# Kernel optimization log

Measured on AMD Instinct MI355X. Metric: run time of the kernel, lower is better.

Reference implementation:

```python
import jax, jax.numpy as jnp
import numpy as np

DIM = 256
NHEADS = 4
HID = 512
B, H, W = 8, 48, 48
EPS = 1e-5


def _ln(x, g, b):
    mu = x.mean(-1, keepdims=True)
    var = ((x - mu) ** 2).mean(-1, keepdims=True)
    return (x - mu) * jax.lax.rsqrt(var + EPS) * g + b


def _mha(x, key_mask, wi, bi, wo, bo):
    # torch nn.MultiheadAttention (batch_first) with key padding restricted to active tokens
    Bn, N, C = x.shape
    hd = C // NHEADS
    qkv = x @ wi.T + bi  # [B,N,3C]
    q, k, v = jnp.split(qkv, 3, axis=-1)
    sh = lambda t: t.reshape(Bn, N, NHEADS, hd).transpose(0, 2, 1, 3)  # [B,h,N,hd]
    q, k, v = sh(q), sh(k), sh(v)
    scores = jnp.einsum('bhqd,bhkd->bhqk', q, k) / np.float32(np.sqrt(hd))
    scores = jnp.where(key_mask[:, None, None, :], scores, jnp.float32(-1e9))
    attn = jax.nn.softmax(scores, axis=-1)
    out = jnp.einsum('bhqk,bhkd->bhqd', attn, v)
    out = out.transpose(0, 2, 1, 3).reshape(Bn, N, C)
    return out @ wo.T + bo


def _mixer(x, key_mask, ln_g, ln_b, in_w, in_b, out_w, out_b, f1_w, f1_b, f2_w, f2_b):
    # MixerBlock: shared LayerNorm used before attn and before FFN
    xn = _ln(x, ln_g, ln_b)
    x = x + _mha(xn, key_mask, in_w, in_b, out_w, out_b)
    h = _ln(x, ln_g, ln_b)
    h = jax.nn.gelu(h @ f1_w.T + f1_b, approximate=False) @ f2_w.T + f2_b
    return x + h


def _forward(f_ir, f_vis, agent_w1, agent_b1, bn_gamma, bn_beta, bn_mean, bn_var,
             agent_w2, agent_b2, hyp_w1, hyp_b1, hyp_w2, hyp_b2,
             mir_ln_g, mir_ln_b, mir_in_w, mir_in_b, mir_out_w, mir_out_b,
             mir_f1_w, mir_f1_b, mir_f2_w, mir_f2_b,
             mvis_ln_g, mvis_ln_b, mvis_in_w, mvis_in_b, mvis_out_w, mvis_out_b,
             mvis_f1_w, mvis_f1_b, mvis_f2_w, mvis_f2_b, highlight_scale):
    Bn, C, Hh, Ww = f_ir.shape
    N = Hh * Ww
    base = f_ir + f_vis

    # SamplingAgent (1x1 convs as einsum, BatchNorm in eval mode)
    x = jnp.concatenate([f_ir, f_vis], axis=1)  # [B,2C,H,W]
    h = jnp.einsum('oc,bchw->bohw', agent_w1, x) + agent_b1[None, :, None, None]
    h = (h - bn_mean[None, :, None, None]) * jax.lax.rsqrt(bn_var[None, :, None, None] + EPS)
    h = h * bn_gamma[None, :, None, None] + bn_beta[None, :, None, None]
    h = jax.nn.relu(h)
    logits = jnp.einsum('oc,bchw->bohw', agent_w2, h) + agent_b2[None, :, None, None]
    w_driver = jax.nn.sigmoid(logits)  # [B,1,H,W]; eval path: driver = student

    # HyperNetwork threshold
    g = w_driver.mean(axis=(2, 3))  # [B,1]
    t = jax.nn.sigmoid(jax.nn.relu(g @ hyp_w1.T + hyp_b1) @ hyp_w2.T + hyp_b2)  # [B,1]

    wflat = w_driver.reshape(Bn, N)
    soft = jax.nn.sigmoid((wflat - t) * 50.0)  # [B,N]

    # active set: soft_mask > 0.5, fallback to top-64 of weights when too few
    active = soft > 0.5
    count = active.sum(axis=1)
    _, idx64 = jax.lax.top_k(wflat, 64)
    m64 = jnp.zeros((Bn, N), dtype=bool).at[jnp.arange(Bn)[:, None], idx64].set(True)
    active = jnp.where((count >= 64)[:, None], active, m64)

    tok_ir = f_ir.reshape(Bn, C, N).transpose(0, 2, 1)   # [B,N,C]
    tok_vis = f_vis.reshape(Bn, C, N).transpose(0, 2, 1)
    tok_base = base.reshape(Bn, C, N).transpose(0, 2, 1)

    refined_ir = _mixer(tok_ir, active, mir_ln_g, mir_ln_b, mir_in_w, mir_in_b,
                        mir_out_w, mir_out_b, mir_f1_w, mir_f1_b, mir_f2_w, mir_f2_b)
    refined_vis = _mixer(tok_vis, active, mvis_ln_g, mvis_ln_b, mvis_in_w, mvis_in_b,
                         mvis_out_w, mvis_out_b, mvis_f1_w, mvis_f1_b, mvis_f2_w, mvis_f2_b)

    wsel = wflat[..., None]
    fusion = refined_ir * wsel + refined_vis * (1.0 - wsel)
    delta = fusion * soft[..., None]
    mod = 1.0 + soft[..., None] * highlight_scale
    final = jnp.where(active[..., None], (tok_base + delta) * mod, tok_base)  # scatter-back
    f_final = final.transpose(0, 2, 1).reshape(Bn, C, Hh, Ww)
    aux_loss = jnp.float32(0.0)
    return f_final, aux_loss


def setup_inputs() -> dict:
    key = jax.random.key(0)
    ks = jax.random.split(key, 32)
    C = DIM
    S = 0.02
    r = lambda i, shape, s=S: jax.random.normal(ks[i], shape, dtype=jnp.float32) * s

    def mixer_params(prefix, k0):
        return {
            prefix + '_ln_g': jnp.ones((C,), jnp.float32),
            prefix + '_ln_b': jnp.zeros((C,), jnp.float32),
            prefix + '_in_w': r(k0, (3 * C, C)),
            prefix + '_in_b': jnp.zeros((3 * C,), jnp.float32),
            prefix + '_out_w': r(k0 + 1, (C, C)),
            prefix + '_out_b': jnp.zeros((C,), jnp.float32),
            prefix + '_f1_w': r(k0 + 2, (4 * C, C)),
            prefix + '_f1_b': jnp.zeros((4 * C,), jnp.float32),
            prefix + '_f2_w': r(k0 + 3, (C, 4 * C)),
            prefix + '_f2_b': jnp.zeros((C,), jnp.float32),
        }

    inp = {
        'f_ir': jax.random.normal(ks[0], (B, C, H, W), dtype=jnp.float32),
        'f_vis': jax.random.normal(ks[1], (B, C, H, W), dtype=jnp.float32),
        'agent_w1': r(2, (HID, 2 * C)),
        'agent_b1': jnp.zeros((HID,), jnp.float32),
        'bn_gamma': jnp.ones((HID,), jnp.float32),
        'bn_beta': jnp.zeros((HID,), jnp.float32),
        'bn_mean': jnp.zeros((HID,), jnp.float32),
        'bn_var': jnp.ones((HID,), jnp.float32),
        'agent_w2': r(3, (1, HID)),
        'agent_b2': jnp.zeros((1,), jnp.float32),
        'hyp_w1': r(4, (16, 1), 0.5),
        'hyp_b1': jnp.zeros((16,), jnp.float32),
        'hyp_w2': r(5, (1, 16), 0.5),
        'hyp_b2': jnp.zeros((1,), jnp.float32),
        'highlight_scale': jnp.float32(1.0),
    }
    inp.update(mixer_params('mir', 6))
    inp.update(mixer_params('mvis', 10))
    return inp


def reference(f_ir, f_vis, agent_w1, agent_b1, bn_gamma, bn_beta, bn_mean, bn_var,
              agent_w2, agent_b2, hyp_w1, hyp_b1, hyp_w2, hyp_b2,
              mir_ln_g, mir_ln_b, mir_in_w, mir_in_b, mir_out_w, mir_out_b,
              mir_f1_w, mir_f1_b, mir_f2_w, mir_f2_b,
              mvis_ln_g, mvis_ln_b, mvis_in_w, mvis_in_b, mvis_out_w, mvis_out_b,
              mvis_f1_w, mvis_f1_b, mvis_f2_w, mvis_f2_b, highlight_scale):
    return _forward(f_ir, f_vis, agent_w1, agent_b1, bn_gamma, bn_beta, bn_mean, bn_var,
                    agent_w2, agent_b2, hyp_w1, hyp_b1, hyp_w2, hyp_b2,
                    mir_ln_g, mir_ln_b, mir_in_w, mir_in_b, mir_out_w, mir_out_b,
                    mir_f1_w, mir_f1_b, mir_f2_w, mir_f2_b,
                    mvis_ln_g, mvis_ln_b, mvis_in_w, mvis_in_b, mvis_out_w, mvis_out_b,
                    mvis_f1_w, mvis_f1_b, mvis_f2_w, mvis_f2_b, highlight_scale)
```

## Files before the change

### kernel.cpp

```cpp
#include <hip/hip_runtime.h>
#include <hip/hip_bf16.h>
#include <cstdint>
#include <cstddef>

typedef __attribute__((ext_vector_type(8))) short short8;
typedef __attribute__((ext_vector_type(4))) short s16x4;
typedef __attribute__((ext_vector_type(4))) float f32x4;

#define DEVI static __device__ __forceinline__

constexpr int NB   = 8;
constexpr int CDIM = 256;
constexpr int NTOK = 2304;
constexpr int BNT  = NB * NTOK;
constexpr int HIDN = 512;
constexpr int RCAP = 2048;
constexpr size_t BNTC = (size_t)BNT * CDIM;
constexpr size_t KVSTR = (size_t)32 * NTOK * 64;
constexpr size_t HSTR  = (size_t)BNT * 1024;

DEVI unsigned short f2bf(float f) {
  unsigned u = __builtin_bit_cast(unsigned, f);
  unsigned r = 0x7FFFu + ((u >> 16) & 1u);
  return (unsigned short)((u + r) >> 16);
}
DEVI float bf2f(unsigned short h) {
  unsigned u = ((unsigned)h) << 16;
  return __builtin_bit_cast(float, u);
}

__global__ __launch_bounds__(256) void convert_weights(
    const float* __restrict__ miw, const float* __restrict__ mow,
    const float* __restrict__ mf1, const float* __restrict__ mf2,
    const float* __restrict__ viw, const float* __restrict__ vow,
    const float* __restrict__ vf1, const float* __restrict__ vf2,
    unsigned short* __restrict__ dst)
{
  int i = blockIdx.x * 256 + threadIdx.x;
  int m = i / 786432;
  int r = i % 786432;
  const float* src; int off;
  if      (r < 196608) { src = m ? viw : miw; off = r; }
  else if (r < 262144) { src = m ? vow : mow; off = r - 196608; }
  else if (r < 524288) { src = m ? vf1 : mf1; off = r - 262144; }
  else                 { src = m ? vf2 : mf2; off = r - 524288; }
  dst[i] = f2bf(src[off]);
}

__global__ __launch_bounds__(256) void split_w_kernel(
    const float* __restrict__ w1, unsigned short* __restrict__ W2)
{
  int i = blockIdx.x * 256 + threadIdx.x;
  int n = i >> 9, k = i & 511;
  float v = w1[i];
  unsigned short hi = f2bf(v);
  float r1 = v - bf2f(hi);
  unsigned short mid = f2bf(r1);
  size_t base = (size_t)n * 1024 + k;
  W2[base] = hi; W2[base + 512] = mid;
}

__global__ __launch_bounds__(256) void split_x_kernel(
    const float* __restrict__ f_ir, const float* __restrict__ f_vis,
    unsigned short* __restrict__ A2)
{
  __shared__ float tile[64][65];
  int n0 = blockIdx.x * 64, c0 = blockIdx.y * 64, b = blockIdx.z;
  int tid = threadIdx.x;
  const float* src = (c0 < 256) ? f_ir : f_vis;
  int cc0 = c0 & 255;
#pragma unroll
  for (int i = 0; i < 16; ++i) {
    int l = tid + i * 256;
    int r = l >> 6, col = l & 63;
    tile[r][col] = src[((size_t)b * 256 + cc0 + r) * NTOK + n0 + col];
  }
  __syncthreads();
#pragma unroll
  for (int i = 0; i < 16; ++i) {
    int l = tid + i * 256;
    int r = l >> 6, col = l & 63;
    float v = tile[col][r];
    unsigned short hi = f2bf(v);
    float r1 = v - bf2f(hi);
    unsigned short mid = f2bf(r1);
    size_t base = ((size_t)b * NTOK + n0 + r) * 1024 + c0 + col;
    A2[base] = hi; A2[base + 512] = mid;
  }
}

__global__ __launch_bounds__(256) void agent_gemm(
    const unsigned short* __restrict__ A2, const unsigned short* __restrict__ W2,
    const float* __restrict__ b1,
    const float* __restrict__ bng, const float* __restrict__ bnb,
    const float* __restrict__ bnm, const float* __restrict__ bnv,
    const float* __restrict__ w2, float* __restrict__ hpart)
{
  __shared__ unsigned short As[128][72];
  __shared__ unsigned short Ws[128][72];
  __shared__ float scl[64], shl[64], w2l[64];
  int tid = threadIdx.x;
  int lane = tid & 63, wid = tid >> 6;
  int wm = (wid >> 1) * 64, wn = (wid & 1) * 32;
  int m0 = blockIdx.x * 128, n0 = blockIdx.y * 64;
  if (tid < 64) {
    int n = n0 + tid;
    double inv = 1.0 / sqrt((double)bnv[n] + 1e-5);
    double sc = (double)bng[n] * inv;
    scl[tid] = (float)sc;
    shl[tid] = (float)(((double)b1[n] - (double)bnm[n]) * sc + (double)bnb[n]);
    w2l[tid] = w2[n];
  }
  f32x4 zero = {0.f, 0.f, 0.f, 0.f};
  f32x4 acc[4][2];
#pragma unroll
  for (int i = 0; i < 4; ++i)
#pragma unroll
    for (int j = 0; j < 2; ++j) acc[i][j] = zero;

  for (int kin = 0; kin < 512; kin += 64) {
    __syncthreads();
#pragma unroll
    for (int i = 0; i < 4; ++i) {
      int l = tid + i * 256;
      int r = l >> 3, ch = (l & 7) * 8;
      *(short8*)&As[r][ch] = *(const short8*)&A2[(size_t)(m0 + r) * 1024 + kin + ch];
    }
#pragma unroll
    for (int i = 0; i < 4; ++i) {
      int l = tid + i * 256;
      int r = l >> 3, ch = (l & 7) * 8;
      int wr = (r < 64) ? r : (r - 64);
      int wo = (r < 64) ? 0 : 512;
      *(short8*)&Ws[r][ch] = *(const short8*)&W2[(size_t)(n0 + wr) * 1024 + wo + kin + ch];
    }
    __syncthreads();
#pragma unroll
    for (int ks = 0; ks < 2; ++ks) {
      short8 a[4], bh[2], bm[2];
#pragma unroll
      for (int i = 0; i < 4; ++i)
        a[i] = *(const short8*)&As[wm + i * 16 + (lane & 15)][ks * 32 + (lane >> 4) * 8];
#pragma unroll
      for (int j = 0; j < 2; ++j) {
        bh[j] = *(const short8*)&Ws[wn + j * 16 + (lane & 15)][ks * 32 + (lane >> 4) * 8];
        bm[j] = *(const short8*)&Ws[64 + wn + j * 16 + (lane & 15)][ks * 32 + (lane >> 4) * 8];
      }
#pragma unroll
      for (int i = 0; i < 4; ++i)
#pragma unroll
        for (int j = 0; j < 2; ++j) {
          acc[i][j] = __builtin_amdgcn_mfma_f32_16x16x32_bf16(a[i], bh[j], acc[i][j], 0, 0, 0);
          acc[i][j] = __builtin_amdgcn_mfma_f32_16x16x32_bf16(a[i], bm[j], acc[i][j], 0, 0, 0);
        }
    }
  }
  for (int kin = 0; kin < 512; kin += 64) {
    __syncthreads();
#pragma unroll
    for (int i = 0; i < 4; ++i) {
      int l = tid + i * 256;
      int r = l >> 3, ch = (l & 7) * 8;
      *(short8*)&As[r][ch] = *(const short8*)&A2[(size_t)(m0 + r) * 1024 + 512 + kin + ch];
    }
#pragma unroll
    for (int i = 0; i < 2; ++i) {
      int l = tid + i * 256;
      int r = l >> 3, ch = (l & 7) * 8;
      *(short8*)&Ws[r][ch] = *(const short8*)&W2[(size_t)(n0 + r) * 1024 + kin + ch];
    }
    __syncthreads();
#pragma unroll
    for (int ks = 0; ks < 2; ++ks) {
      short8 a[4], bh[2];
#pragma unroll
      for (int i = 0; i < 4; ++i)
        a[i] = *(const short8*)&As[wm + i * 16 + (lane & 15)][ks * 32 + (lane >> 4) * 8];
#pragma unroll
      for (int j = 0; j < 2; ++j)
        bh[j] = *(const short8*)&Ws[wn + j * 16 + (lane & 15)][ks * 32 + (lane >> 4) * 8];
#pragma unroll
      for (int i = 0; i < 4; ++i)
#pragma unroll
        for (int j = 0; j < 2; ++j)
          acc[i][j] = __builtin_amdgcn_mfma_f32_16x16x32_bf16(a[i], bh[j], acc[i][j], 0, 0, 0);
    }
  }

  int rbase = (lane >> 4) * 4;
  int cbase = lane & 15;
  float part[4][4];
#pragma unroll
  for (int i = 0; i < 4; ++i) {
#pragma unroll
    for (int r = 0; r < 4; ++r) {
      float p = 0.f;
#pragma unroll
      for (int j = 0; j < 2; ++j) {
        int nl = wn + j * 16 + cbase;
        float val = acc[i][j][r] * scl[nl] + shl[nl];
        if (val > 0.f) p += val * w2l[nl];
      }
      part[i][r] = p;
    }
  }
#pragma unroll
  for (int msk = 1; msk < 16; msk <<= 1) {
#pragma unroll
    for (int i = 0; i < 4; ++i)
#pragma unroll
      for (int r = 0; r < 4; ++r)
        part[i][r] += __shfl_xor(part[i][r], msk);
  }
  if (cbase == 0) {
    int slot = blockIdx.y * 2 + (wid & 1);
#pragma unroll
    for (int i = 0; i < 4; ++i)
#pragma unroll
      for (int r = 0; r < 4; ++r) {
        int mm = m0 + wm + i * 16 + rbase + r;
        hpart[(size_t)mm * 16 + slot] = part[i][r];
      }
  }
}

__global__ __launch_bounds__(256) void agent2_finish(
    const float* __restrict__ hpart, const float* __restrict__ b2,
    double* __restrict__ w64out, float* __restrict__ w32out)
{
  int pix = blockIdx.x * 256 + threadIdx.x;
  const float* hp = hpart + (size_t)pix * 16;
  double s = (double)b2[0];
#pragma unroll
  for (int j = 0; j < 16; ++j) s += (double)hp[j];
  double wd = 1.0 / (1.0 + exp(-s));
  w64out[pix] = wd;
  w32out[pix] = (float)wd;
}

__global__ __launch_bounds__(256) void hyper_kernel(
    const double* __restrict__ w64, const float* __restrict__ hw1,
    const float* __restrict__ hb1, const float* __restrict__ hw2,
    const float* __restrict__ hb2, double* __restrict__ t64)
{
  __shared__ double red[256];
  int b = blockIdx.x, tid = threadIdx.x;
  double s = 0.0;
  for (int i = tid; i < NTOK; i += 256) s += w64[(size_t)b * NTOK + i];
  red[tid] = s;
  __syncthreads();
  for (int st = 128; st; st >>= 1) {
    if (tid < st) red[tid] += red[tid + st];
    __syncthreads();
  }
  if (tid == 0) {
    double g = red[0] / 2304.0;
    double acc = (double)hb2[0];
    for (int j = 0; j < 16; ++j) {
      double hh = g * (double)hw1[j] + (double)hb1[j];
      hh = hh > 0.0 ? hh : 0.0;
      acc += hh * (double)hw2[j];
    }
    t64[b] = 1.0 / (1.0 + exp(-acc));
  }
}

__global__ __launch_bounds__(256) void flag_kernel(
    const double* __restrict__ w64, const double* __restrict__ t64,
    int* __restrict__ rcount, int* __restrict__ rlist)
{
  int i = blockIdx.x * 256 + threadIdx.x;
  int b = i / NTOK;
  if (fabs(w64[i] - t64[b]) < 2e-4) {
    int idx = atomicAdd(rcount, 1);
    if (idx < RCAP) rlist[idx] = i;
  }
}

__global__ __launch_bounds__(256) void refine_kernel(
    const float* __restrict__ f_ir, const float* __restrict__ f_vis,
    const float* __restrict__ w1, const float* __restrict__ b1,
    const float* __restrict__ bng, const float* __restrict__ bnb,
    const float* __restrict__ bnm, const float* __restrict__ bnv,
    const float* __restrict__ w2, const float* __restrict__ b2,
    const int* __restrict__ rlist, const int* __restrict__ rcount,
    double* __restrict__ w64, float* __restrict__ w32)
{
  int nr = rcount[0]; if (nr > RCAP) nr = RCAP;
  if ((int)blockIdx.x >= nr) return;
  int pix = rlist[blockIdx.x];
  int b = pix / NTOK, n = pix % NTOK;
  __shared__ double xs[512];
  __shared__ double scs[512], shs[512];
  __shared__ double lred[4];
  int tid = threadIdx.x, lane = tid & 63, wid = tid >> 6;
  xs[tid]       = (double)f_ir [((size_t)b * 256 + tid) * NTOK + n];
  xs[256 + tid] = (double)f_vis[((size_t)b * 256 + tid) * NTOK + n];
#pragma unroll
  for (int h = 0; h < 2; ++h) {
    int o = tid + h * 256;
    double inv = 1.0 / sqrt((double)bnv[o] + 1e-5);
    double sc = (double)bng[o] * inv;
    scs[o] = sc;
    shs[o] = ((double)b1[o] - (double)bnm[o]) * sc + (double)bnb[o];
  }
  __syncthreads();
  double xp[8];
#pragma unroll
  for (int j = 0; j < 8; ++j) xp[j] = xs[lane * 8 + j];
  double lg = 0.0;
  for (int oo = 0; oo < 128; oo += 8) {
    int o = wid * 128 + oo;
    double s[8] = {0, 0, 0, 0, 0, 0, 0, 0};
    const float* wr = w1 + (size_t)o * 512 + lane * 8;
#pragma unroll
    for (int t = 0; t < 8; ++t) {
#pragma unroll
      for (int j = 0; j < 8; ++j)
        s[t] += (double)wr[t * 512 + j] * xp[j];
    }
#pragma unroll
    for (int m = 1; m < 64; m <<= 1) {
#pragma unroll
      for (int t = 0; t < 8; ++t) s[t] += __shfl_xor(s[t], m);
    }
#pragma unroll
    for (int t = 0; t < 8; ++t) {
      int ot = o + t;
      double hv = s[t] * scs[ot] + shs[ot];
      if (hv > 0.0) lg += hv * (double)w2[ot];
    }
  }
  if (lane == 0) lred[wid] = lg;
  __syncthreads();
  if (tid == 0) {
    double L = lred[0] + lred[1] + lred[2] + lred[3] + (double)b2[0];
    double wd = 1.0 / (1.0 + exp(-L));
    w64[pix] = wd;
    w32[pix] = (float)wd;
  }
}

__global__ __launch_bounds__(256) void mask_kernel(
    const double* __restrict__ w64, const double* __restrict__ t64,
    float* __restrict__ soft, int* __restrict__ active, int* __restrict__ count)
{
  __shared__ int wred[4];
  int tid = threadIdx.x;
  int i = blockIdx.x * 256 + tid;
  int b = blockIdx.x / 9;
  double z = (w64[i] - t64[b]) * 50.0;
  double sd = 1.0 / (1.0 + exp(-z));
  soft[i] = (float)sd;
  int a = sd > 0.5 ? 1 : 0;
  active[i] = a;
  unsigned long long ball = __ballot(a);
  if ((tid & 63) == 0) wred[tid >> 6] = __popcll(ball);
  __syncthreads();
  if (tid == 0)
    atomicAdd(&count[b], wred[0] + wred[1] + wred[2] + wred[3]);
}

__global__ __launch_bounds__(256) void compact_kernel(
    const double* __restrict__ w64, const int* __restrict__ count,
    int* __restrict__ active, int* __restrict__ actidx,
    int* __restrict__ invmap, int* __restrict__ nact, int* __restrict__ npad)
{
  __shared__ double wv[NTOK];
  __shared__ double rv[256];
  __shared__ int   ri[256];
  __shared__ int wtot[9][4];
  int b = blockIdx.x, tid = threadIdx.x, lane = tid & 63, wid = tid >> 6;

  if (count[b] < 64) {
    for (int i = tid; i < NTOK; i += 256) {
      wv[i] = w64[(size_t)b * NTOK + i];
      active[(size_t)b * NTOK + i] = 0;
    }
    __syncthreads();
    for (int it = 0; it < 64; ++it) {
      double best = -1e300; int bi = 1 << 30;
      for (int i = tid; i < NTOK; i += 256) {
        double vvv = wv[i];
        if (vvv > best || (vvv == best && i < bi)) { best = vvv; bi = i; }
      }
      rv[tid] = best; ri[tid] = bi;
      __syncthreads();
      for (int st = 128; st; st >>= 1) {
        if (tid < st) {
          if (rv[tid + st] > rv[tid] ||
              (rv[tid + st] == rv[tid] && ri[tid + st] < ri[tid])) {
            rv[tid] = rv[tid + st]; ri[tid] = ri[tid + st];
          }
        }
        __syncthreads();
      }
      if (tid == 0) { active[(size_t)b * NTOK + ri[0]] = 1; wv[ri[0]] = -1e300; }
      __syncthreads();
    }
  }
  __syncthreads();

  unsigned long long ltmask = (1ull << lane) - 1ull;
  int sbase = 0;
  for (int c = 0; c < 9; ++c) {
    int i = c * 256 + tid;
    int a = active[(size_t)b * NTOK + i];
    unsigned long long ball = __ballot(a);
    int wpre = __popcll(ball & ltmask);
    if (lane == 0) wtot[c][wid] = __popcll(ball);
    __syncthreads();
    int cross = 0;
    for (int w = 0; w < wid; ++w) cross += wtot[c][w];
    int slot = sbase + cross + wpre;
    if (a) actidx[(size_t)b * NTOK + slot] = i;
    invmap[(size_t)b * NTOK + i] = a ? slot : -1;
    sbase += wtot[c][0] + wtot[c][1] + wtot[c][2] + wtot[c][3];
  }
  int n = sbase;
  int np = (n + 127) & ~127;
  if (np > NTOK) np = NTOK;
  for (int i = n + tid; i < np; i += 256) actidx[(size_t)b * NTOK + i] = -1;
  if (tid == 0) { nact[b] = n; npad[b] = np; }
}

__global__ __launch_bounds__(256) void gather_kernel(
    const unsigned short* __restrict__ A2, const int* __restrict__ actidx,
    const int* __restrict__ npad, float* __restrict__ xc)
{
  int b = blockIdx.y, i0 = blockIdx.x * 64, z = blockIdx.z;
  int cofs = z * 256;
  xc += (size_t)z * BNTC;
  if (i0 >= npad[b]) return;
  __shared__ int idx[64];
  int tid = threadIdx.x;
  if (tid < 64) idx[tid] = actidx[(size_t)b * NTOK + i0 + tid];
  __syncthreads();
#pragma unroll
  for (int it = 0; it < 16; ++it) {
    int s = tid + it * 256;
    int r = s >> 6, q4 = (s & 63) * 4;
    int src = idx[r];
    f32x4 v = {0.f, 0.f, 0.f, 0.f};
    if (src >= 0) {
      const unsigned short* p = A2 + ((size_t)b * NTOK + src) * 1024 + cofs + q4;
      s16x4 hi = *(const s16x4*)&p[0];
      s16x4 md = *(const s16x4*)&p[512];
#pragma unroll
      for (int j = 0; j < 4; ++j)
        v[j] = bf2f((unsigned short)hi[j]) + bf2f((unsigned short)md[j]);
    }
    *(f32x4*)&xc[((size_t)b * NTOK + i0 + r) * 256 + q4] = v;
  }
}

__global__ __launch_bounds__(256) void ln_kernel(
    const float* __restrict__ x, size_t xstr,
    const float* __restrict__ g0, const float* __restrict__ be0,
    const float* __restrict__ g1, const float* __restrict__ be1, int zbase,
    unsigned short* __restrict__ out, size_t ostr, const int* __restrict__ npad)
{
  int z = blockIdx.y;
  x += (size_t)z * xstr; out += (size_t)z * ostr;
  const float* gamma = ((zbase + z) & 1) ? g1 : g0;
  const float* beta  = ((zbase + z) & 1) ? be1 : be0;
  int lane = threadIdx.x & 63, wid = threadIdx.x >> 6;
  int tok = blockIdx.x * 4 + wid;
  int b = tok / NTOK;
  if ((tok - b * NTOK) >= npad[b]) return;
  const float* xp = x + (size_t)tok * 256;
  f32x4 v = *(const f32x4*)&xp[lane * 4];
  float s = v[0] + v[1] + v[2] + v[3];
#pragma unroll
  for (int m = 1; m < 64; m <<= 1) s += __shfl_xor(s, m);
  float mu = s * (1.f / 256.f);
  float vs = 0.f;
#pragma unroll
  for (int j = 0; j < 4; ++j) { float d = v[j] - mu; vs += d * d; }
#pragma unroll
  for (int m = 1; m < 64; m <<= 1) vs += __shfl_xor(vs, m);
  float rs = rsqrtf(vs * (1.f / 256.f) + 1e-5f);
  f32x4 gg = *(const f32x4*)&gamma[lane * 4];
  f32x4 bb = *(const f32x4*)&beta[lane * 4];
  unsigned short r0 = f2bf((v[0] - mu) * rs * gg[0] + bb[0]);
  unsigned short r1 = f2bf((v[1] - mu) * rs * gg[1] + bb[1]);
  unsigned short r2 = f2bf((v[2] - mu) * rs * gg[2] + bb[2]);
  unsigned short r3 = f2bf((v[3] - mu) * rs * gg[3] + bb[3]);
  uint2 pk;
  pk.x = (unsigned)r0 | ((unsigned)r1 << 16);
  pk.y = (unsigned)r2 | ((unsigned)r3 << 16);
  *(uint2*)&out[(size_t)tok * 256 + lane * 4] = pk;
}

template <int EPI>
__global__ __launch_bounds__(256) void gemm_bt(
    const unsigned short* __restrict__ A, size_t astr,
    const unsigned short* __restrict__ Wt, size_t wstr,
    const float* __restrict__ biasA, const float* __restrict__ biasB, int zbase,
    float* __restrict__ xres, size_t xstr,
    float* __restrict__ fout, size_t fstr,
    unsigned short* __restrict__ bout, size_t bstr,
    unsigned short* __restrict__ qb, unsigned short* __restrict__ kb,
    unsigned short* __restrict__ vtb, size_t qstr,
    const int* __restrict__ npad, int N, int K)
{
  int z = blockIdx.z;
  A += (size_t)z * astr;
  Wt += (size_t)z * wstr;
  const float* bias = ((zbase + z) & 1) ? biasB : biasA;
  if (EPI == 0) { qb += (size_t)z * qstr; kb += (size_t)z * qstr; vtb += (size_t)z * qstr; }
  if (EPI == 1 || EPI == 3) xres += (size_t)z * xstr;
  if (EPI == 3) fout += (size_t)z * fstr;
  if (EPI == 2) bout += (size_t)z * bstr;

  int m0 = blockIdx.x * 128, n0 = blockIdx.y * 128;
  int bb = m0 / NTOK;
  if ((m0 - bb * NTOK) >= npad[bb]) return;
  __shared__ unsigned short As[128][72];
  __shared__ unsigned short Ws[128][72];
  int tid = threadIdx.x;
  int lane = tid & 63, wid = tid >> 6;
  int wm = (wid >> 1) * 64, wn = (wid & 1) * 64;
  f32x4 zero = {0.f, 0.f, 0.f, 0.f};
  f32x4 acc[4][4];
#pragma unroll
  for (int i = 0; i < 4; ++i)
#pragma unroll
    for (int j = 0; j < 4; ++j) acc[i][j] = zero;

  for (int kc = 0; kc < K; kc += 64) {
#pragma unroll
    for (int i = 0; i < 4; ++i) {
      int l = tid + i * 256;
      int r = l >> 3, ch = (l & 7) * 8;
      *(short8*)&As[r][ch] = *(const short8*)&A[(size_t)(m0 + r) * K + kc + ch];
      *(short8*)&Ws[r][ch] = *(const short8*)&Wt[(size_t)(n0 + r) * K + kc + ch];
    }
    __syncthreads();
#pragma unroll
    for (int ks = 0; ks < 2; ++ks) {
      short8 a[4], bf[4];
#pragma unroll
      for (int i = 0; i < 4; ++i)
        a[i] = *(const short8*)&As[wm + i * 16 + (lane & 15)][ks * 32 + (lane >> 4) * 8];
#pragma unroll
      for (int j = 0; j < 4; ++j)
        bf[j] = *(const short8*)&Ws[wn + j * 16 + (lane & 15)][ks * 32 + (lane >> 4) * 8];
#pragma unroll
      for (int i = 0; i < 4; ++i)
#pragma unroll
        for (int j = 0; j < 4; ++j)
          acc[i][j] = __builtin_amdgcn_mfma_f32_16x16x32_bf16(a[i], bf[j], acc[i][j], 0, 0, 0);
    }
    __syncthreads();
  }

  int rbase = (lane >> 4) * 4;
  int cbase = lane & 15;
  if (EPI == 0) {
#pragma unroll
    for (int i = 0; i < 4; ++i) {
#pragma unroll
      for (int j = 0; j < 4; ++j) {
        int n = n0 + wn + j * 16 + cbase;
        int sect = n >> 8, hh = (n & 255) >> 6, d = n & 63;
        int mA = m0 + wm + i * 16 + rbase;
        int b = mA / NTOK, tok0 = mA % NTOK;
        size_t bh = (size_t)(b * 4 + hh);
        float vals[4];
#pragma unroll
        for (int r = 0; r < 4; ++r) vals[r] = acc[i][j][r] + bias[n];
        if (sect == 0) {
#pragma unroll
          for (int r = 0; r < 4; ++r)
            qb[(bh * NTOK + tok0 + r) * 64 + d] = f2bf(vals[r] * 0.125f);
        } else if (sect == 1) {
#pragma unroll
          for (int r = 0; r < 4; ++r)
            kb[(bh * NTOK + tok0 + r) * 64 + d] = f2bf(vals[r]);
        } else {
          unsigned short p0 = f2bf(vals[0]), p1 = f2bf(vals[1]);
          unsigned short p2 = f2bf(vals[2]), p3 = f2bf(vals[3]);
          uint2 pk;
          pk.x = (unsigned)p0 | ((unsigned)p1 << 16);
          pk.y = (unsigned)p2 | ((unsigned)p3 << 16);
          *(uint2*)&vtb[(bh * 64 + d) * NTOK + tok0] = pk;
        }
      }
    }
  } else {
#pragma unroll
    for (int i = 0; i < 4; ++i) {
#pragma unroll
      for (int j = 0; j < 4; ++j) {
#pragma unroll
        for (int r = 0; r < 4; ++r) {
          int m = m0 + wm + i * 16 + rbase + r;
          int n = n0 + wn + j * 16 + cbase;
          float v = acc[i][j][r] + bias[n];
          size_t idx = (size_t)m * N + n;
          if (EPI == 1) {
            xres[idx] += v;
          } else if (EPI == 2) {
            float g = 0.5f * v * (1.f + erff(v * 0.70710678118654752f));
            bout[idx] = f2bf(g);
          } else {
            fout[idx] = xres[idx] + v;
          }
        }
      }
    }
  }
}

__global__ __launch_bounds__(256) void flash_kernel(
    const unsigned short* __restrict__ Q, const unsigned short* __restrict__ Kt,
    const unsigned short* __restrict__ VT, const int* __restrict__ nact,
    const int* __restrict__ npad, unsigned short* __restrict__ attnout)
{
  int z = blockIdx.z;
  Q += (size_t)z * KVSTR; Kt += (size_t)z * KVSTR; VT += (size_t)z * KVSTR;
  attnout += (size_t)z * BNTC;
  int bh = blockIdx.x, qt = blockIdx.y;
  int b = bh >> 2, h = bh & 3;
  int np = npad[b], na = nact[b];
  if (qt * 64 >= np) return;
  __shared__ unsigned short Ks[64][72];
  __shared__ unsigned short Vs[64][72];
  __shared__ unsigned short Ps[4][16][72];
  __shared__ float madd[64];
  int tid = threadIdx.x, lane = tid & 63, wid = tid >> 6;
  int qrow = qt * 64 + wid * 16 + (lane & 15);
  const unsigned short* qptr = Q + ((size_t)bh * NTOK + qrow) * 64;
  short8 aq0 = *(const short8*)&qptr[(lane >> 4) * 8];
  short8 aq1 = *(const short8*)&qptr[32 + (lane >> 4) * 8];
  f32x4 zero = {0.f, 0.f, 0.f, 0.f};
  f32x4 o[4];
  float mrow[4], lrow[4];
#pragma unroll
  for (int n = 0; n < 4; ++n) o[n] = zero;
#pragma unroll
  for (int r = 0; r < 4; ++r) { mrow[r] = -INFINITY; lrow[r] = 0.f; }
  const unsigned short* kbase = Kt + (size_t)bh * NTOK * 64;
  const unsigned short* vbase = VT + (size_t)bh * 64 * NTOK;
  int nkt = (na + 63) >> 6;

  for (int kt = 0; kt < nkt; ++kt) {
    int k0 = kt * 64;
#pragma unroll
    for (int i = 0; i < 2; ++i) {
      int l = tid + i * 256;
      int r = l >> 3, ch = (l & 7) * 8;
      *(short8*)&Ks[r][ch] = *(const short8*)&kbase[(size_t)(k0 + r) * 64 + ch];
      *(short8*)&Vs[r][ch] = *(const short8*)&vbase[(size_t)r * NTOK + k0 + ch];
    }
    if (tid < 64) madd[tid] = (k0 + tid < na) ? 0.f : -1e9f;
    __syncthreads();

    f32x4 s[4];
#pragma unroll
    for (int n = 0; n < 4; ++n) s[n] = zero;
#pragma unroll
    for (int n = 0; n < 4; ++n) {
      short8 bk0 = *(const short8*)&Ks[n * 16 + (lane & 15)][(lane >> 4) * 8];
      short8 bk1 = *(const short8*)&Ks[n * 16 + (lane & 15)][32 + (lane >> 4) * 8];
      s[n] = __builtin_amdgcn_mfma_f32_16x16x32_bf16(aq0, bk0, s[n], 0, 0, 0);
      s[n] = __builtin_amdgcn_mfma_f32_16x16x32_bf16(aq1, bk1, s[n], 0, 0, 0);
    }
    float pm[4] = {-INFINITY, -INFINITY, -INFINITY, -INFINITY};
#pragma unroll
    for (int n = 0; n < 4; ++n) {
      float ca = madd[n * 16 + (lane & 15)];
#pragma unroll
      for (int r = 0; r < 4; ++r) {
        s[n][r] += ca;
        pm[r] = fmaxf(pm[r], s[n][r]);
      }
    }
#pragma unroll
    for (int r = 0; r < 4; ++r) {
#pragma unroll
      for (int msk = 1; msk < 16; msk <<= 1)
        pm[r] = fmaxf(pm[r], __shfl_xor(pm[r], msk));
    }
    float sf[4], psum[4];
#pragma unroll
    for (int r = 0; r < 4; ++r) {
      float mn = fmaxf(mrow[r], pm[r]);
      sf[r] = __expf(mrow[r] - mn);
      mrow[r] = mn;
      psum[r] = 0.f;
    }
#pragma unroll
    for (int n = 0; n < 4; ++n)
#pragma unroll
      for (int r = 0; r < 4; ++r) {
        float p = __expf(s[n][r] - mrow[r]);
        s[n][r] = p;
        psum[r] += p;
      }
#pragma unroll
    for (int r = 0; r < 4; ++r) {
#pragma unroll
      for (int msk = 1; msk < 16; msk <<= 1)
        psum[r] += __shfl_xor(psum[r], msk);
      lrow[r] = lrow[r] * sf[r] + psum[r];
    }
#pragma unroll
    for (int n = 0; n < 4; ++n)
#pragma unroll
      for (int r = 0; r < 4; ++r) o[n][r] *= sf[r];
#pragma unroll
    for (int n = 0; n < 4; ++n)
#pragma unroll
      for (int r = 0; r < 4; ++r)
        Ps[wid][(lane >> 4) * 4 + r][n * 16 + (lane & 15)] = f2bf(s[n][r]);
    asm volatile("s_waitcnt lgkmcnt(0)" ::: "memory");
    __builtin_amdgcn_sched_barrier(0);
    short8 ap0 = *(const short8*)&Ps[wid][lane & 15][(lane >> 4) * 8];
    short8 ap1 = *(const short8*)&Ps[wid][lane & 15][32 + (lane >> 4) * 8];
#pragma unroll
    for (int n = 0; n < 4; ++n) {
      short8 bv0 = *(const short8*)&Vs[n * 16 + (lane & 15)][(lane >> 4) * 8];
      short8 bv1 = *(const short8*)&Vs[n * 16 + (lane & 15)][32 + (lane >> 4) * 8];
      o[n] = __builtin_amdgcn_mfma_f32_16x16x32_bf16(ap0, bv0, o[n], 0, 0, 0);
      o[n] = __builtin_amdgcn_mfma_f32_16x16x32_bf16(ap1, bv1, o[n], 0, 0, 0);
    }
    __syncthreads();
  }
#pragma unroll
  for (int n = 0; n < 4; ++n)
#pragma unroll
    for (int r = 0; r < 4; ++r) {
      int row = qt * 64 + wid * 16 + (lane >> 4) * 4 + r;
      int col = h * 64 + n * 16 + (lane & 15);
      float v = o[n][r] / lrow[r];
      attnout[((size_t)b * NTOK + row) * 256 + col] = f2bf(v);
    }
}

__global__ __launch_bounds__(256) void final_kernel(
    const float* __restrict__ f_ir, const float* __restrict__ f_vis,
    const float* __restrict__ rirc, const float* __restrict__ rvisc,
    const float* __restrict__ w32, const float* __restrict__ soft,
    const int* __restrict__ invmap, const float* __restrict__ hs_ptr,
    float* __restrict__ out)
{
  __shared__ float tir[64][65], tvis[64][65];
  __shared__ float wl[64], sl[64];
  __shared__ int il[64];
  int n0 = blockIdx.x * 64, c0 = blockIdx.y * 64, b = blockIdx.z;
  int tid = threadIdx.x;
  float hs = hs_ptr[0];
  if (tid < 64) {
    int t = b * NTOK + n0 + tid;
    wl[tid] = w32[t]; sl[tid] = soft[t]; il[tid] = invmap[t];
  }
  __syncthreads();
#pragma unroll
  for (int i = 0; i < 16; ++i) {
    int l = tid + i * 256;
    int r = l >> 6, col = l & 63;
    int ci = il[r];
    if (ci >= 0) {
      size_t idx = ((size_t)b * NTOK + ci) * 256 + c0 + col;
      tir[r][col] = rirc[idx];
      tvis[r][col] = rvisc[idx];
    }
  }
  __syncthreads();
#pragma unroll
  for (int i = 0; i < 16; ++i) {
    int l = tid + i * 256;
    int r = l >> 6, col = l & 63;
    size_t gidx = ((size_t)b * 256 + c0 + r) * NTOK + n0 + col;
    float base = f_ir[gidx] + f_vis[gidx];
    float val;
    if (il[col] >= 0) {
      float ww = wl[col], ss = sl[col];
      float fusion = tir[col][r] * ww + tvis[col][r] * (1.f - ww);
      val = (base + fusion * ss) * (1.f + ss * hs);
    } else {
      val = base;
    }
    out[gidx] = val;
  }
  if (blockIdx.x == 0 && blockIdx.y == 0 && blockIdx.z == 0 && tid == 0)
    out[(size_t)NB * 256 * NTOK] = 0.f;
}

extern "C" void kernel_launch(void* const* d_in, const int* in_sizes, int n_in,
                              void* d_out, int out_size, void* d_ws, size_t ws_size,
                              hipStream_t stream)
{
  const float* f_ir     = (const float*)d_in[0];
  const float* f_vis    = (const float*)d_in[1];
  const float* agent_w1 = (const float*)d_in[2];
  const float* agent_b1 = (const float*)d_in[3];
  const float* bn_gamma = (const float*)d_in[4];
  const float* bn_beta  = (const float*)d_in[5];
  const float* bn_mean  = (const float*)d_in[6];
  const float* bn_var   = (const float*)d_in[7];
  const float* agent_w2 = (const float*)d_in[8];
  const float* agent_b2 = (const float*)d_in[9];
  const float* hyp_w1   = (const float*)d_in[10];
  const float* hyp_b1   = (const float*)d_in[11];
  const float* hyp_w2   = (const float*)d_in[12];
  const float* hyp_b2   = (const float*)d_in[13];
  int hs_idx = (in_sizes[14] == 1) ? 14 : 34;
  int mix0   = (in_sizes[14] == 1) ? 15 : 14;
  const float* hs_ptr = (const float*)d_in[hs_idx];
  const float* mir_ln_g = (const float*)d_in[mix0 + 0];
  const float* mir_ln_b = (const float*)d_in[mix0 + 1];
  const float* mir_in_w = (const float*)d_in[mix0 + 2];
  const float* mir_in_b = (const float*)d_in[mix0 + 3];
  const float* mir_out_w= (const float*)d_in[mix0 + 4];
  const float* mir_out_b= (const float*)d_in[mix0 + 5];
  const float* mir_f1_w = (const float*)d_in[mix0 + 6];
  const float* mir_f1_b = (const float*)d_in[mix0 + 7];
  const float* mir_f2_w = (const float*)d_in[mix0 + 8];
  const float* mir_f2_b = (const float*)d_in[mix0 + 9];
  const float* mvis_ln_g = (const float*)d_in[mix0 + 10];
  const float* mvis_ln_b = (const float*)d_in[mix0 + 11];
  const float* mvis_in_w = (const float*)d_in[mix0 + 12];
  const float* mvis_in_b = (const float*)d_in[mix0 + 13];
  const float* mvis_out_w= (const float*)d_in[mix0 + 14];
  const float* mvis_out_b= (const float*)d_in[mix0 + 15];
  const float* mvis_f1_w = (const float*)d_in[mix0 + 16];
  const float* mvis_f1_b = (const float*)d_in[mix0 + 17];
  const float* mvis_f2_w = (const float*)d_in[mix0 + 18];
  const float* mvis_f2_b = (const float*)d_in[mix0 + 19];

  auto padded = [](size_t bytes) { return (bytes + 255) & ~(size_t)255; };
  size_t need2 = padded(2 * BNTC * 4)
               + padded(2 * BNTC * 2)
               + 3 * padded(2 * KVSTR * 2)
               + padded(2 * BNTC * 2)
               + padded(2 * BNTC * 4)
               + padded((size_t)2 * 786432 * 2)
               + padded((size_t)512 * 1024 * 2)
               + padded((size_t)BNT * 16 * 4)
               + padded((size_t)BNT * 8)
               + padded(64) + padded(64)
               + 3 * padded((size_t)BNT * 4)
               + padded((size_t)RCAP * 4)
               + 2 * padded((size_t)BNT * 4)
               + 2 * padded(64);
  int zc = (ws_size >= need2 + (1 << 20)) ? 2 : 1;

  char* ws = (char*)d_ws;
  size_t off = 0;
  auto alloc = [&](size_t bytes) {
    size_t o = off;
    off = (off + bytes + 255) & ~(size_t)255;
    return o;
  };
  size_t o_xc    = alloc(2 * BNTC * 4);
  size_t o_xn    = alloc((size_t)zc * BNTC * 2);
  size_t o_q     = alloc((size_t)zc * KVSTR * 2);
  size_t o_k     = alloc((size_t)zc * KVSTR * 2);
  size_t o_vt    = alloc((size_t)zc * KVSTR * 2);
  size_t o_attn  = alloc((size_t)zc * BNTC * 2);
  size_t o_rr    = alloc(2 * BNTC * 4);
  size_t o_wbf   = alloc((size_t)2 * 786432 * 2);
  size_t o_w2s   = alloc((size_t)512 * 1024 * 2);
  size_t o_hp    = alloc((size_t)BNT * 16 * 4);
  size_t o_w64   = alloc((size_t)BNT * 8);
  size_t o_t64   = alloc(64);
  size_t o_count = alloc(64);
  size_t o_w32   = alloc((size_t)BNT * 4);
  size_t o_soft  = alloc((size_t)BNT * 4);
  size_t o_act   = alloc((size_t)BNT * 4);
  size_t o_rlist = alloc((size_t)RCAP * 4);
  size_t o_aidx  = alloc((size_t)BNT * 4);
  size_t o_inv   = alloc((size_t)BNT * 4);
  size_t o_nact  = alloc(64);
  size_t o_npad  = alloc(64);
  (void)n_in; (void)out_size;

  float*  xc   = (float*)(ws + o_xc);
  unsigned short* xn   = (unsigned short*)(ws + o_xn);
  unsigned short* q    = (unsigned short*)(ws + o_q);
  unsigned short* k    = (unsigned short*)(ws + o_k);
  unsigned short* vt   = (unsigned short*)(ws + o_vt);
  unsigned short* attn = (unsigned short*)(ws + o_attn);
  unsigned short* hffn = (unsigned short*)(ws + o_q);
  float*  rr   = (float*)(ws + o_rr);
  unsigned short* A2 = (unsigned short*)(ws + o_rr);
  unsigned short* wbf  = (unsigned short*)(ws + o_wbf);
  unsigned short* W2   = (unsigned short*)(ws + o_w2s);
  float*  hpart = (float*)(ws + o_hp);
  double* w64  = (double*)(ws + o_w64);
  double* t64  = (double*)(ws + o_t64);
  int*    cnt  = (int*)(ws + o_count);
  int*    rcount = cnt + 8;
  float*  w32  = (float*)(ws + o_w32);
  float*  soft = (float*)(ws + o_soft);
  int*    act  = (int*)(ws + o_act);
  int*    rlist = (int*)(ws + o_rlist);
  int*    aidx = (int*)(ws + o_aidx);
  int*    invm = (int*)(ws + o_inv);
  int*    nact = (int*)(ws + o_nact);
  int*    npad = (int*)(ws + o_npad);

  const unsigned short* mir_in  = wbf;
  const unsigned short* mir_out = wbf + 196608;
  const unsigned short* mir_f1  = wbf + 262144;
  const unsigned short* mir_f2  = wbf + 524288;
  const unsigned short* vis_in  = wbf + 786432;
  const unsigned short* vis_out = wbf + 786432 + 196608;
  const unsigned short* vis_f1  = wbf + 786432 + 262144;
  const unsigned short* vis_f2  = wbf + 786432 + 524288;

  convert_weights<<<6144, 256, 0, stream>>>(mir_in_w, mir_out_w, mir_f1_w, mir_f2_w,
                                            mvis_in_w, mvis_out_w, mvis_f1_w, mvis_f2_w,
                                            wbf);
  split_w_kernel<<<1024, 256, 0, stream>>>(agent_w1, W2);
  split_x_kernel<<<dim3(36, 8, 8), 256, 0, stream>>>(f_ir, f_vis, A2);

  agent_gemm<<<dim3(BNT / 128, 8), 256, 0, stream>>>(
      A2, W2, agent_b1, bn_gamma, bn_beta, bn_mean, bn_var, agent_w2, hpart);
  agent2_finish<<<BNT / 256, 256, 0, stream>>>(hpart, agent_b2, w64, w32);
  hyper_kernel<<<8, 256, 0, stream>>>(w64, hyp_w1, hyp_b1, hyp_w2, hyp_b2, t64);
  hipMemsetAsync(cnt, 0, 16 * sizeof(int), stream);
  flag_kernel<<<BNT / 256, 256, 0, stream>>>(w64, t64, rcount, rlist);
  refine_kernel<<<RCAP, 256, 0, stream>>>(
      f_ir, f_vis, agent_w1, agent_b1, bn_gamma, bn_beta, bn_mean, bn_var,
      agent_w2, agent_b2, rlist, rcount, w64, w32);
  mask_kernel<<<BNT / 256, 256, 0, stream>>>(w64, t64, soft, act, cnt);
  compact_kernel<<<8, 256, 0, stream>>>(w64, cnt, act, aidx, invm, nact, npad);

  gather_kernel<<<dim3(36, 8, 2), 256, 0, stream>>>(A2, aidx, npad, xc);

  if (zc == 2) {
    size_t WSTR = 786432;
    ln_kernel<<<dim3(BNT / 4, 2), 256, 0, stream>>>(
        xc, BNTC, mir_ln_g, mir_ln_b, mvis_ln_g, mvis_ln_b, 0, xn, BNTC, npad);
    gemm_bt<0><<<dim3(BNT / 128, 6, 2), 256, 0, stream>>>(
        xn, BNTC, mir_in, WSTR, mir_in_b, mvis_in_b, 0,
        nullptr, 0, nullptr, 0, nullptr, 0, q, k, vt, KVSTR, npad, 768, 256);
    flash_kernel<<<dim3(32, 36, 2), 256, 0, stream>>>(q, k, vt, nact, npad, attn);
    gemm_bt<1><<<dim3(BNT / 128, 2, 2), 256, 0, stream>>>(
        attn, BNTC, mir_out, WSTR, mir_out_b, mvis_out_b, 0,
        xc, BNTC, nullptr, 0, nullptr, 0, nullptr, nullptr, nullptr, 0, npad, 256, 256);
    ln_kernel<<<dim3(BNT / 4, 2), 256, 0, stream>>>(
        xc, BNTC, mir_ln_g, mir_ln_b, mvis_ln_g, mvis_ln_b, 0, xn, BNTC, npad);
    gemm_bt<2><<<dim3(BNT / 128, 8, 2), 256, 0, stream>>>(
        xn, BNTC, mir_f1, WSTR, mir_f1_b, mvis_f1_b, 0,
        nullptr, 0, nullptr, 0, hffn, HSTR, nullptr, nullptr, nullptr, 0, npad, 1024, 256);
    gemm_bt<3><<<dim3(BNT / 128, 2, 2), 256, 0, stream>>>(
        hffn, HSTR, mir_f2, WSTR, mir_f2_b, mvis_f2_b, 0,
        xc, BNTC, rr, BNTC, nullptr, 0, nullptr, nullptr, nullptr, 0, npad, 256, 1024);
  } else {
    for (int s = 0; s < 2; ++s) {
      const float* g   = s ? mvis_ln_g : mir_ln_g;
      const float* be  = s ? mvis_ln_b : mir_ln_b;
      const unsigned short* w_in  = s ? vis_in  : mir_in;
      const unsigned short* w_out = s ? vis_out : mir_out;
      const unsigned short* w_f1  = s ? vis_f1  : mir_f1;
      const unsigned short* w_f2  = s ? vis_f2  : mir_f2;
      const float* b_in  = s ? mvis_in_b  : mir_in_b;
      const float* b_out = s ? mvis_out_b : mir_out_b;
      const float* b_f1  = s ? mvis_f1_b  : mir_f1_b;
      const float* b_f2  = s ? mvis_f2_b  : mir_f2_b;
      float* xcs = xc + (size_t)s * BNTC;
      float* rrs = rr + (size_t)s * BNTC;
      ln_kernel<<<dim3(BNT / 4, 1), 256, 0, stream>>>(
          xcs, 0, g, be, g, be, 0, xn, 0, npad);
      gemm_bt<0><<<dim3(BNT / 128, 6, 1), 256, 0, stream>>>(
          xn, 0, w_in, 0, b_in, b_in, 0,
          nullptr, 0, nullptr, 0, nullptr, 0, q, k, vt, 0, npad, 768, 256);
      flash_kernel<<<dim3(32, 36, 1), 256, 0, stream>>>(q, k, vt, nact, npad, attn);
      gemm_bt<1><<<dim3(BNT / 128, 2, 1), 256, 0, stream>>>(
          attn, 0, w_out, 0, b_out, b_out, 0,
          xcs, 0, nullptr, 0, nullptr, 0, nullptr, nullptr, nullptr, 0, npad, 256, 256);
      ln_kernel<<<dim3(BNT / 4, 1), 256, 0, stream>>>(
          xcs, 0, g, be, g, be, 0, xn, 0, npad);
      gemm_bt<2><<<dim3(BNT / 128, 8, 1), 256, 0, stream>>>(
          xn, 0, w_f1, 0, b_f1, b_f1, 0,
          nullptr, 0, nullptr, 0, hffn, 0, nullptr, nullptr, nullptr, 0, npad, 1024, 256);
      gemm_bt<3><<<dim3(BNT / 128, 2, 1), 256, 0, stream>>>(
          hffn, 0, w_f2, 0, b_f2, b_f2, 0,
          xcs, 0, rrs, 0, nullptr, 0, nullptr, nullptr, nullptr, 0, npad, 256, 1024);
    }
  }

  final_kernel<<<dim3(36, 4, 8), 256, 0, stream>>>(
      f_ir, f_vis, rr, rr + BNTC, w32, soft, invm, hs_ptr, (float*)d_out);
}
```

Measured before the change: 267.3 us.

## Drop split-bf16 input precision, fuse agent finish/hyper/flag and mask/compact kernels

The input activations are now stored as a single bf16 value instead of a hi+mid pair. This halves the A2 buffer and removes the second K pass in the agent GEMM. To make up for the lost precision, the refine tolerance window is widened and the refine capacity is doubled, so more borderline pixels are recomputed exactly. The sigmoid finish, hypernet threshold and flagging steps are fused into one per-batch kernel, and the mask step is folded into compaction, which cuts several launches. The risks are that the gather now feeds the mixers bf16-rounded inputs, and that the larger refine launch adds cost.

```diff
diff --git a/kernel.cpp b/kernel.cpp
--- a/kernel.cpp
+++ b/kernel.cpp
@@ -14,7 +14,7 @@
 constexpr int NTOK = 2304;
 constexpr int BNT  = NB * NTOK;
 constexpr int HIDN = 512;
-constexpr int RCAP = 2048;
+constexpr int RCAP = 4096;
 constexpr size_t BNTC = (size_t)BNT * CDIM;
 constexpr size_t KVSTR = (size_t)32 * NTOK * 64;
 constexpr size_t HSTR  = (size_t)BNT * 1024;
@@ -80,12 +80,7 @@
   for (int i = 0; i < 16; ++i) {
     int l = tid + i * 256;
     int r = l >> 6, col = l & 63;
-    float v = tile[col][r];
-    unsigned short hi = f2bf(v);
-    float r1 = v - bf2f(hi);
-    unsigned short mid = f2bf(r1);
-    size_t base = ((size_t)b * NTOK + n0 + r) * 1024 + c0 + col;
-    A2[base] = hi; A2[base + 512] = mid;
+    A2[((size_t)b * NTOK + n0 + r) * 512 + c0 + col] = f2bf(tile[col][r]);
   }
 }
 
@@ -124,7 +119,7 @@
     for (int i = 0; i < 4; ++i) {
       int l = tid + i * 256;
       int r = l >> 3, ch = (l & 7) * 8;
-      *(short8*)&As[r][ch] = *(const short8*)&A2[(size_t)(m0 + r) * 1024 + kin + ch];
+      *(short8*)&As[r][ch] = *(const short8*)&A2[(size_t)(m0 + r) * 512 + kin + ch];
     }
 #pragma unroll
     for (int i = 0; i < 4; ++i) {
@@ -155,37 +150,6 @@
         }
     }
   }
-  for (int kin = 0; kin < 512; kin += 64) {
-    __syncthreads();
-#pragma unroll
-    for (int i = 0; i < 4; ++i) {
-      int l = tid + i * 256;
-      int r = l >> 3, ch = (l & 7) * 8;
-      *(short8*)&As[r][ch] = *(const short8*)&A2[(size_t)(m0 + r) * 1024 + 512 + kin + ch];
-    }
-#pragma unroll
-    for (int i = 0; i < 2; ++i) {
-      int l = tid + i * 256;
-      int r = l >> 3, ch = (l & 7) * 8;
-      *(short8*)&Ws[r][ch] = *(const short8*)&W2[(size_t)(n0 + r) * 1024 + kin + ch];
-    }
-    __syncthreads();
-#pragma unroll
-    for (int ks = 0; ks < 2; ++ks) {
-      short8 a[4], bh[2];
-#pragma unroll
-      for (int i = 0; i < 4; ++i)
-        a[i] = *(const short8*)&As[wm + i * 16 + (lane & 15)][ks * 32 + (lane >> 4) * 8];
-#pragma unroll
-      for (int j = 0; j < 2; ++j)
-        bh[j] = *(const short8*)&Ws[wn + j * 16 + (lane & 15)][ks * 32 + (lane >> 4) * 8];
-#pragma unroll
-      for (int i = 0; i < 4; ++i)
-#pragma unroll
-        for (int j = 0; j < 2; ++j)
-          acc[i][j] = __builtin_amdgcn_mfma_f32_16x16x32_bf16(a[i], bh[j], acc[i][j], 0, 0, 0);
-    }
-  }
 
   int rbase = (lane >> 4) * 4;
   int cbase = lane & 15;
@@ -224,29 +188,30 @@
   }
 }
 
-__global__ __launch_bounds__(256) void agent2_finish(
+__global__ __launch_bounds__(256) void decide_kernel(
     const float* __restrict__ hpart, const float* __restrict__ b2,
-    double* __restrict__ w64out, float* __restrict__ w32out)
-{
-  int pix = blockIdx.x * 256 + threadIdx.x;
-  const float* hp = hpart + (size_t)pix * 16;
-  double s = (double)b2[0];
-#pragma unroll
-  for (int j = 0; j < 16; ++j) s += (double)hp[j];
-  double wd = 1.0 / (1.0 + exp(-s));
-  w64out[pix] = wd;
-  w32out[pix] = (float)wd;
-}
-
-__global__ __launch_bounds__(256) void hyper_kernel(
-    const double* __restrict__ w64, const float* __restrict__ hw1,
-    const float* __restrict__ hb1, const float* __restrict__ hw2,
-    const float* __restrict__ hb2, double* __restrict__ t64)
+    const float* __restrict__ hw1, const float* __restrict__ hb1,
+    const float* __restrict__ hw2, const float* __restrict__ hb2,
+    double* __restrict__ w64, float* __restrict__ w32, double* __restrict__ t64,
+    int* __restrict__ rcount, int* __restrict__ rlist)
 {
   __shared__ double red[256];
+  __shared__ double tsh;
   int b = blockIdx.x, tid = threadIdx.x;
+  double wloc[9];
   double s = 0.0;
-  for (int i = tid; i < NTOK; i += 256) s += w64[(size_t)b * NTOK + i];
+#pragma unroll
+  for (int c = 0; c < 9; ++c) {
+    int pix = b * NTOK + c * 256 + tid;
+    const float* hp = hpart + (size_t)pix * 16;
+    double lg = (double)b2[0];
+#pragma unroll
+    for (int j = 0; j < 16; ++j) lg += (double)hp[j];
+    double wd = 1.0 / (1.0 + exp(-lg));
+    w64[pix] = wd; w32[pix] = (float)wd;
+    wloc[c] = wd;
+    s += wd;
+  }
   red[tid] = s;
   __syncthreads();
   for (int st = 128; st; st >>= 1) {
@@ -261,19 +226,18 @@
       hh = hh > 0.0 ? hh : 0.0;
       acc += hh * (double)hw2[j];
     }
-    t64[b] = 1.0 / (1.0 + exp(-acc));
-  }
-}
-
-__global__ __launch_bounds__(256) void flag_kernel(
-    const double* __restrict__ w64, const double* __restrict__ t64,
-    int* __restrict__ rcount, int* __restrict__ rlist)
-{
-  int i = blockIdx.x * 256 + threadIdx.x;
-  int b = i / NTOK;
-  if (fabs(w64[i] - t64[b]) < 2e-4) {
-    int idx = atomicAdd(rcount, 1);
-    if (idx < RCAP) rlist[idx] = i;
+    tsh = 1.0 / (1.0 + exp(-acc));
+    t64[b] = tsh;
+  }
+  __syncthreads();
+  double t = tsh;
+#pragma unroll
+  for (int c = 0; c < 9; ++c) {
+    if (fabs(wloc[c] - t) < 1.5e-3) {
+      int pix = b * NTOK + c * 256 + tid;
+      int idx = atomicAdd(rcount, 1);
+      if (idx < RCAP) rlist[idx] = pix;
+    }
   }
 }
 
@@ -341,29 +305,9 @@
   }
 }
 
-__global__ __launch_bounds__(256) void mask_kernel(
+__global__ __launch_bounds__(256) void compact_kernel(
     const double* __restrict__ w64, const double* __restrict__ t64,
-    float* __restrict__ soft, int* __restrict__ active, int* __restrict__ count)
-{
-  __shared__ int wred[4];
-  int tid = threadIdx.x;
-  int i = blockIdx.x * 256 + tid;
-  int b = blockIdx.x / 9;
-  double z = (w64[i] - t64[b]) * 50.0;
-  double sd = 1.0 / (1.0 + exp(-z));
-  soft[i] = (float)sd;
-  int a = sd > 0.5 ? 1 : 0;
-  active[i] = a;
-  unsigned long long ball = __ballot(a);
-  if ((tid & 63) == 0) wred[tid >> 6] = __popcll(ball);
-  __syncthreads();
-  if (tid == 0)
-    atomicAdd(&count[b], wred[0] + wred[1] + wred[2] + wred[3]);
-}
-
-__global__ __launch_bounds__(256) void compact_kernel(
-    const double* __restrict__ w64, const int* __restrict__ count,
-    int* __restrict__ active, int* __restrict__ actidx,
+    float* __restrict__ soft, int* __restrict__ active, int* __restrict__ actidx,
     int* __restrict__ invmap, int* __restrict__ nact, int* __restrict__ npad)
 {
   __shared__ double wv[NTOK];
@@ -371,8 +315,30 @@
   __shared__ int   ri[256];
   __shared__ int wtot[9][4];
   int b = blockIdx.x, tid = threadIdx.x, lane = tid & 63, wid = tid >> 6;
-
-  if (count[b] < 64) {
+  double t = t64[b];
+  unsigned long long ltmask = (1ull << lane) - 1ull;
+
+  int sbase = 0;
+  for (int c = 0; c < 9; ++c) {
+    int i = c * 256 + tid;
+    double wd = w64[(size_t)b * NTOK + i];
+    double sd = 1.0 / (1.0 + exp(-(wd - t) * 50.0));
+    soft[(size_t)b * NTOK + i] = (float)sd;
+    int a = sd > 0.5 ? 1 : 0;
+    active[(size_t)b * NTOK + i] = a;
+    unsigned long long ball = __ballot(a);
+    int wpre = __popcll(ball & ltmask);
+    if (lane == 0) wtot[c][wid] = __popcll(ball);
+    __syncthreads();
+    int cross = 0;
+    for (int w = 0; w < wid; ++w) cross += wtot[c][w];
+    int slot = sbase + cross + wpre;
+    if (a) actidx[(size_t)b * NTOK + slot] = i;
+    invmap[(size_t)b * NTOK + i] = a ? slot : -1;
+    sbase += wtot[c][0] + wtot[c][1] + wtot[c][2] + wtot[c][3];
+  }
+
+  if (sbase < 64) {
     for (int i = tid; i < NTOK; i += 256) {
       wv[i] = w64[(size_t)b * NTOK + i];
       active[(size_t)b * NTOK + i] = 0;
@@ -398,24 +364,21 @@
       if (tid == 0) { active[(size_t)b * NTOK + ri[0]] = 1; wv[ri[0]] = -1e300; }
       __syncthreads();
     }
-  }
-  __syncthreads();
-
-  unsigned long long ltmask = (1ull << lane) - 1ull;
-  int sbase = 0;
-  for (int c = 0; c < 9; ++c) {
-    int i = c * 256 + tid;
-    int a = active[(size_t)b * NTOK + i];
-    unsigned long long ball = __ballot(a);
-    int wpre = __popcll(ball & ltmask);
-    if (lane == 0) wtot[c][wid] = __popcll(ball);
-    __syncthreads();
-    int cross = 0;
-    for (int w = 0; w < wid; ++w) cross += wtot[c][w];
-    int slot = sbase + cross + wpre;
-    if (a) actidx[(size_t)b * NTOK + slot] = i;
-    invmap[(size_t)b * NTOK + i] = a ? slot : -1;
-    sbase += wtot[c][0] + wtot[c][1] + wtot[c][2] + wtot[c][3];
+    sbase = 0;
+    for (int c = 0; c < 9; ++c) {
+      int i = c * 256 + tid;
+      int a = active[(size_t)b * NTOK + i];
+      unsigned long long ball = __ballot(a);
+      int wpre = __popcll(ball & ltmask);
+      if (lane == 0) wtot[c][wid] = __popcll(ball);
+      __syncthreads();
+      int cross = 0;
+      for (int w = 0; w < wid; ++w) cross += wtot[c][w];
+      int slot = sbase + cross + wpre;
+      if (a) actidx[(size_t)b * NTOK + slot] = i;
+      invmap[(size_t)b * NTOK + i] = a ? slot : -1;
+      sbase += wtot[c][0] + wtot[c][1] + wtot[c][2] + wtot[c][3];
+    }
   }
   int n = sbase;
   int np = (n + 127) & ~127;
@@ -443,12 +406,11 @@
     int src = idx[r];
     f32x4 v = {0.f, 0.f, 0.f, 0.f};
     if (src >= 0) {
-      const unsigned short* p = A2 + ((size_t)b * NTOK + src) * 1024 + cofs + q4;
+      const unsigned short* p = A2 + ((size_t)b * NTOK + src) * 512 + cofs + q4;
       s16x4 hi = *(const s16x4*)&p[0];
-      s16x4 md = *(const s16x4*)&p[512];
 #pragma unroll
       for (int j = 0; j < 4; ++j)
-        v[j] = bf2f((unsigned short)hi[j]) + bf2f((unsigned short)md[j]);
+        v[j] = bf2f((unsigned short)hi[j]);
     }
     *(f32x4*)&xc[((size_t)b * NTOK + i0 + r) * 256 + q4] = v;
   }
@@ -912,6 +874,7 @@
   const unsigned short* vis_f1  = wbf + 786432 + 262144;
   const unsigned short* vis_f2  = wbf + 786432 + 524288;
 
+  hipMemsetAsync(cnt, 0, 16 * sizeof(int), stream);
   convert_weights<<<6144, 256, 0, stream>>>(mir_in_w, mir_out_w, mir_f1_w, mir_f2_w,
                                             mvis_in_w, mvis_out_w, mvis_f1_w, mvis_f2_w,
                                             wbf);
@@ -920,15 +883,12 @@
 
   agent_gemm<<<dim3(BNT / 128, 8), 256, 0, stream>>>(
       A2, W2, agent_b1, bn_gamma, bn_beta, bn_mean, bn_var, agent_w2, hpart);
-  agent2_finish<<<BNT / 256, 256, 0, stream>>>(hpart, agent_b2, w64, w32);
-  hyper_kernel<<<8, 256, 0, stream>>>(w64, hyp_w1, hyp_b1, hyp_w2, hyp_b2, t64);
-  hipMemsetAsync(cnt, 0, 16 * sizeof(int), stream);
-  flag_kernel<<<BNT / 256, 256, 0, stream>>>(w64, t64, rcount, rlist);
+  decide_kernel<<<8, 256, 0, stream>>>(
+      hpart, agent_b2, hyp_w1, hyp_b1, hyp_w2, hyp_b2, w64, w32, t64, rcount, rlist);
   refine_kernel<<<RCAP, 256, 0, stream>>>(
       f_ir, f_vis, agent_w1, agent_b1, bn_gamma, bn_beta, bn_mean, bn_var,
       agent_w2, agent_b2, rlist, rcount, w64, w32);
-  mask_kernel<<<BNT / 256, 256, 0, stream>>>(w64, t64, soft, act, cnt);
-  compact_kernel<<<8, 256, 0, stream>>>(w64, cnt, act, aidx, invm, nact, npad);
+  compact_kernel<<<8, 256, 0, stream>>>(w64, t64, soft, act, aidx, invm, nact, npad);
 
   gather_kernel<<<dim3(36, 8, 2), 256, 0, stream>>>(A2, aidx, npad, xc);
 
```

Measured after the change: 267.0 us. About the same (-0.1%).
